# Optimization experiments

Hardware: AMD Instinct MI355X
Metric: run time of the kernel (lower is better)

Reference implementation:

```python
import jax, jax.numpy as jnp
import numpy as np

N_NODES = 50000


def _gin_aggregate(x, src, dst):
    # sum_{j in N(i)} x_j via scatter-add over edges; eps=0 so add self term
    msg = x[src]  # [E, d]
    return x + jax.ops.segment_sum(msg, dst, num_segments=N_NODES)


def _mlp(h, Wa, ba, Wb, bb):
    return jax.nn.relu(h @ Wa + ba) @ Wb + bb


def setup_inputs() -> dict:
    key = jax.random.key(0)
    ks = jax.random.split(key, 12)
    d_in, d_h, n_cls, n_edges = 128, 128, 40, 800000
    x = jax.random.normal(ks[0], (N_NODES, d_in), dtype=jnp.float32)
    edge_index = jax.random.randint(ks[1], (2, n_edges), 0, N_NODES, dtype=jnp.int64)
    s = lambda k, sh: jax.random.normal(k, sh, dtype=jnp.float32) / np.sqrt(sh[0])
    return {
        "x": x,
        "edge_index": edge_index,
        "W11": s(ks[2], (d_in, 2 * d_h)), "b11": jnp.zeros((2 * d_h,), jnp.float32),
        "W12": s(ks[3], (2 * d_h, d_h)), "b12": jnp.zeros((d_h,), jnp.float32),
        "W21": s(ks[4], (d_h, 2 * d_h)), "b21": jnp.zeros((2 * d_h,), jnp.float32),
        "W22": s(ks[5], (2 * d_h, d_h)), "b22": jnp.zeros((d_h,), jnp.float32),
        "Wfc": s(ks[6], (d_h, n_cls)), "bfc": jnp.zeros((n_cls,), jnp.float32),
    }


def reference(x, edge_index, W11, b11, W12, b12, W21, b21, W22, b22, Wfc, bfc):
    src, dst = edge_index[0], edge_index[1]
    # GINConv 1: aggregate then MLP, followed by ReLU
    h = _mlp(_gin_aggregate(x, src, dst), W11, b11, W12, b12)
    h = jax.nn.relu(h)
    # GINConv 2
    h = _mlp(_gin_aggregate(h, src, dst), W21, b21, W22, b22)
    h = jax.nn.relu(h)
    # final classifier
    return h @ Wfc + bfc
```

## Files before the change

kernel.cpp:

```cpp
#include <hip/hip_runtime.h>

#define N_NODES 50000
#define N_EDGES 800000
#define NBUCK   98
#define EPB     8192

typedef __attribute__((ext_vector_type(8))) short short8;
typedef __attribute__((ext_vector_type(4))) float floatx4;

__device__ __forceinline__ float b2f(unsigned short u) {
    union { unsigned int i; float f; } v;
    v.i = ((unsigned int)u) << 16;
    return v.f;
}
__device__ __forceinline__ float ubits(unsigned int b) {
    union { unsigned int i; float f; } v;
    v.i = b;
    return v.f;
}
__device__ __forceinline__ unsigned short f2b(float f) {
    union { float f; unsigned int i; } v;
    v.f = f;
    unsigned int r = v.i + 0x7FFFu + ((v.i >> 16) & 1u);
    return (unsigned short)(r >> 16);
}

__global__ __launch_bounds__(256) void bhist_kernel(const int* __restrict__ dstv,
                                                    int* __restrict__ bkt_cnt) {
    __shared__ int h[NBUCK];
    const int tid = threadIdx.x;
    for (int i = tid; i < NBUCK; i += 256) h[i] = 0;
    __syncthreads();
    const int e0 = blockIdx.x * 1024;
#pragma unroll
    for (int j = 0; j < 4; ++j) {
        int e = e0 + j * 256 + tid;
        if (e < N_EDGES) atomicAdd(&h[dstv[e] >> 9], 1);
    }
    __syncthreads();
    for (int i = tid; i < NBUCK; i += 256)
        if (h[i]) atomicAdd(&bkt_cnt[i], h[i]);
}

__global__ __launch_bounds__(128) void bscan_kernel(const int* __restrict__ bkt_cnt,
                                                    int* __restrict__ bbase,
                                                    int* __restrict__ bcur) {
    __shared__ int s[128];
    const int t = threadIdx.x;
    const int v = (t < NBUCK) ? bkt_cnt[t] : 0;
    s[t] = v;
    __syncthreads();
    for (int off = 1; off < 128; off <<= 1) {
        int u = (t >= off) ? s[t - off] : 0;
        __syncthreads();
        s[t] += u;
        __syncthreads();
    }
    if (t == 0) bbase[0] = 0;
    if (t < NBUCK) {
        bbase[t + 1] = s[t];
        bcur[t] = s[t] - v;
    }
}

__global__ __launch_bounds__(256) void bucket_scatter(const int* __restrict__ srcv,
                                                      const int* __restrict__ dstv,
                                                      int* __restrict__ bcur,
                                                      int* __restrict__ tmp) {
    __shared__ int hist[NBUCK];
    __shared__ int base[NBUCK];
    const int tid = threadIdx.x;
    const int e0 = blockIdx.x * EPB;
    for (int i = tid; i < NBUCK; i += 256) hist[i] = 0;
    __syncthreads();
#pragma unroll 4
    for (int j = 0; j < EPB / 256; ++j) {
        int e = e0 + j * 256 + tid;
        if (e < N_EDGES) atomicAdd(&hist[dstv[e] >> 9], 1);
    }
    __syncthreads();
    for (int i = tid; i < NBUCK; i += 256) {
        base[i] = atomicAdd(&bcur[i], hist[i]);
        hist[i] = 0;
    }
    __syncthreads();
#pragma unroll 4
    for (int j = 0; j < EPB / 256; ++j) {
        int e = e0 + j * 256 + tid;
        if (e < N_EDGES) {
            int d = dstv[e];
            int b = d >> 9;
            int r = atomicAdd(&hist[b], 1);
            tmp[base[b] + r] = srcv[e] | ((d & 511) << 16);
        }
    }
}

__global__ __launch_bounds__(256) void bucket_sort_ex(const int* __restrict__ bbase,
                                                      const int* __restrict__ tmp,
                                                      int* __restrict__ e_src,
                                                      int* __restrict__ row_ptr) {
    __shared__ int cnt[512];
    __shared__ int ps[256];
    __shared__ int buf[12288];
    const int tid = threadIdx.x;
    const int b = blockIdx.x;
    const int nb = b << 9;
    const int rbase = bbase[b], rend = bbase[b + 1];
    const int S = rend - rbase;

    for (int i = tid; i < 512; i += 256) cnt[i] = 0;
    __syncthreads();
    for (int e = tid; e < S; e += 256)
        atomicAdd(&cnt[(tmp[rbase + e] >> 16) & 511], 1);
    __syncthreads();

    const int c0 = cnt[2 * tid], c1 = cnt[2 * tid + 1];
    ps[tid] = c0 + c1;
    __syncthreads();
    for (int off = 1; off < 256; off <<= 1) {
        int u = (tid >= off) ? ps[tid - off] : 0;
        __syncthreads();
        ps[tid] += u;
        __syncthreads();
    }
    const int off0 = ps[tid] - (c0 + c1);
    const int off1 = off0 + c0;
    cnt[2 * tid] = off0;
    cnt[2 * tid + 1] = off1;
    if (nb + 2 * tid < N_NODES)     row_ptr[nb + 2 * tid] = rbase + off0;
    if (nb + 2 * tid + 1 < N_NODES) row_ptr[nb + 2 * tid + 1] = rbase + off1;
    if (b == NBUCK - 1 && tid == 0) row_ptr[N_NODES] = N_EDGES;
    __syncthreads();

    for (int e = tid; e < S; e += 256) {
        int p = tmp[rbase + e];
        int dl = (p >> 16) & 511;
        int pos = atomicAdd(&cnt[dl], 1);
        buf[pos] = p & 0xFFFF;
    }
    __syncthreads();
    for (int i = tid; i < S; i += 256) e_src[rbase + i] = buf[i];
}

__global__ void prep_kernel(const float* __restrict__ x,
                            const float* __restrict__ W11, const float* __restrict__ W12,
                            const float* __restrict__ W21, const float* __restrict__ W22,
                            const float* __restrict__ Wfc,
                            unsigned short* __restrict__ xb,
                            unsigned short* __restrict__ Wt11, unsigned short* __restrict__ Wt12,
                            unsigned short* __restrict__ Wt21, unsigned short* __restrict__ Wt22,
                            unsigned short* __restrict__ Wfct,
                            int* __restrict__ bkt_cnt) {
    int bid = blockIdx.x;
    if (bid < 512) {
        int which = bid >> 7;
        int idx = (bid & 127) * 256 + threadIdx.x;
        const float* W = (which == 0) ? W11 : (which == 1) ? W12 : (which == 2) ? W21 : W22;
        unsigned short* Wt = (which == 0) ? Wt11 : (which == 1) ? Wt12 : (which == 2) ? Wt21 : Wt22;
        int K = (which & 1) ? 256 : 128;
        int N = (which & 1) ? 128 : 256;
        int k = idx / N, n = idx - k * N;
        Wt[n * K + k] = f2b(W[idx]);
    } else if (bid < 536) {
        int idx = (bid - 512) * 256 + threadIdx.x;
        int n = idx >> 7, k = idx & 127;
        Wfct[idx] = (n < 40) ? f2b(Wfc[k * 40 + n]) : (unsigned short)0;
    } else if (bid < 3661) {
        int i = (bid - 536) * 256 + threadIdx.x;
        const float4 a = *reinterpret_cast<const float4*>(x + (size_t)i * 8);
        const float4 b = *reinterpret_cast<const float4*>(x + (size_t)i * 8 + 4);
        ushort4 u0, u1;
        u0.x = f2b(a.x); u0.y = f2b(a.y); u0.z = f2b(a.z); u0.w = f2b(a.w);
        u1.x = f2b(b.x); u1.y = f2b(b.y); u1.z = f2b(b.z); u1.w = f2b(b.w);
        *reinterpret_cast<ushort4*>(xb + (size_t)i * 8) = u0;
        *reinterpret_cast<ushort4*>(xb + (size_t)i * 8 + 4) = u1;
    } else {
        if (threadIdx.x < NBUCK) bkt_cnt[threadIdx.x] = 0;
    }
}

__global__ __launch_bounds__(256) void agg_bf16q(const unsigned short* __restrict__ X,
                                                 const int* __restrict__ row_ptr,
                                                 const int* __restrict__ e_src,
                                                 unsigned short* __restrict__ agg) {
    const int node = (blockIdx.x * 256 + threadIdx.x) >> 6;
    const int lane = threadIdx.x & 63;
    const int qw = lane >> 4, ql = lane & 15;
    const size_t off = (size_t)ql * 8;

    const int beg = row_ptr[node], end = row_ptr[node + 1];
    float acc[8];
#pragma unroll
    for (int k = 0; k < 8; ++k) acc[k] = 0.f;

    if (qw == 0) {
        uint4 u = *reinterpret_cast<const uint4*>(X + (size_t)node * 128 + off);
        const unsigned int* up = (const unsigned int*)&u;
#pragma unroll
        for (int k = 0; k < 4; ++k) {
            acc[2 * k]     += ubits(up[k] << 16);
            acc[2 * k + 1] += ubits(up[k] & 0xFFFF0000u);
        }
    }

    int e = beg + qw;
    for (; e + 12 < end; e += 16) {
        const int s0 = e_src[e], s1 = e_src[e + 4], s2 = e_src[e + 8], s3 = e_src[e + 12];
        uint4 u0 = *reinterpret_cast<const uint4*>(X + (size_t)s0 * 128 + off);
        uint4 u1 = *reinterpret_cast<const uint4*>(X + (size_t)s1 * 128 + off);
        uint4 u2 = *reinterpret_cast<const uint4*>(X + (size_t)s2 * 128 + off);
        uint4 u3 = *reinterpret_cast<const uint4*>(X + (size_t)s3 * 128 + off);
        const unsigned int* p0 = (const unsigned int*)&u0;
        const unsigned int* p1 = (const unsigned int*)&u1;
        const unsigned int* p2 = (const unsigned int*)&u2;
        const unsigned int* p3 = (const unsigned int*)&u3;
#pragma unroll
        for (int k = 0; k < 4; ++k) {
            acc[2 * k]     += ubits(p0[k] << 16) + ubits(p1[k] << 16)
                            + ubits(p2[k] << 16) + ubits(p3[k] << 16);
            acc[2 * k + 1] += ubits(p0[k] & 0xFFFF0000u) + ubits(p1[k] & 0xFFFF0000u)
                            + ubits(p2[k] & 0xFFFF0000u) + ubits(p3[k] & 0xFFFF0000u);
        }
    }
    for (; e + 4 < end; e += 8) {
        const int s0 = e_src[e], s1 = e_src[e + 4];
        uint4 u0 = *reinterpret_cast<const uint4*>(X + (size_t)s0 * 128 + off);
        uint4 u1 = *reinterpret_cast<const uint4*>(X + (size_t)s1 * 128 + off);
        const unsigned int* p0 = (const unsigned int*)&u0;
        const unsigned int* p1 = (const unsigned int*)&u1;
#pragma unroll
        for (int k = 0; k < 4; ++k) {
            acc[2 * k]     += ubits(p0[k] << 16) + ubits(p1[k] << 16);
            acc[2 * k + 1] += ubits(p0[k] & 0xFFFF0000u) + ubits(p1[k] & 0xFFFF0000u);
        }
    }
    if (e < end) {
        const int s = e_src[e];
        uint4 u = *reinterpret_cast<const uint4*>(X + (size_t)s * 128 + off);
        const unsigned int* p = (const unsigned int*)&u;
#pragma unroll
        for (int k = 0; k < 4; ++k) {
            acc[2 * k]     += ubits(p[k] << 16);
            acc[2 * k + 1] += ubits(p[k] & 0xFFFF0000u);
        }
    }

#pragma unroll
    for (int k = 0; k < 8; ++k) acc[k] += __shfl_xor(acc[k], 32);
#pragma unroll
    for (int k = 0; k < 8; ++k) acc[k] += __shfl_xor(acc[k], 16);

    if (qw == 0) {
        ushort4 o0, o1;
        o0.x = f2b(acc[0]); o0.y = f2b(acc[1]); o0.z = f2b(acc[2]); o0.w = f2b(acc[3]);
        o1.x = f2b(acc[4]); o1.y = f2b(acc[5]); o1.z = f2b(acc[6]); o1.w = f2b(acc[7]);
        unsigned short* p = agg + (size_t)node * 128 + off;
        *reinterpret_cast<ushort4*>(p) = o0;
        *reinterpret_cast<ushort4*>(p + 4) = o1;
    }
}

template <bool FUSE>
__global__ __launch_bounds__(256, FUSE ? 2 : 3) void mlp_fused(
    const unsigned short* __restrict__ X, const unsigned short* __restrict__ Wt1,
    const float* __restrict__ b1, const unsigned short* __restrict__ Wt2,
    const float* __restrict__ b2, unsigned short* __restrict__ Y,
    const unsigned short* __restrict__ Wfct, const float* __restrict__ bfc,
    float* __restrict__ out, int M) {
    __shared__ __align__(16) char smem[FUSE ? 57344 : 52224];
    unsigned short* A   = (unsigned short*)smem;
    unsigned short* B2q = (unsigned short*)smem;
    unsigned short* B1h = (unsigned short*)(smem + 17408);
    unsigned short* T   = (unsigned short*)(smem + 17408);
    unsigned short* Hc  = (unsigned short*)(smem + 52224);

    const int tid = threadIdx.x;
    const int m0 = blockIdx.x * 64;
    const int lane = tid & 63, w = tid >> 6;
    const int qm = lane & 15, quad = lane >> 4;

#pragma unroll
    for (int j = 0; j < 4; ++j) {
        int i = j * 256 + tid;
        int r = i >> 4, c8 = (i & 15) << 3;
        uint4 v = {0, 0, 0, 0};
        if (m0 + r < M) v = *reinterpret_cast<const uint4*>(X + (size_t)(m0 + r) * 128 + c8);
        *reinterpret_cast<uint4*>(&A[r * 136 + c8]) = v;
    }

    floatx4 acc1[2][4][2];
#pragma unroll
    for (int c = 0; c < 2; ++c)
#pragma unroll
        for (int mt = 0; mt < 4; ++mt)
#pragma unroll
            for (int nt = 0; nt < 2; ++nt) acc1[c][mt][nt] = {0.f, 0.f, 0.f, 0.f};

    for (int c = 0; c < 2; ++c) {
#pragma unroll
        for (int j = 0; j < 8; ++j) {
            int i = j * 256 + tid;
            int r = i >> 4, c8 = (i & 15) << 3;
            *reinterpret_cast<uint4*>(&B1h[r * 136 + c8]) =
                *reinterpret_cast<const uint4*>(Wt1 + (size_t)(c * 128 + r) * 128 + c8);
        }
        __syncthreads();
#pragma unroll
        for (int ks = 0; ks < 4; ++ks) {
            const int kb = ks * 32 + quad * 8;
            short8 a[4], b[2];
#pragma unroll
            for (int mt = 0; mt < 4; ++mt)
                a[mt] = *reinterpret_cast<const short8*>(&A[(mt * 16 + qm) * 136 + kb]);
#pragma unroll
            for (int nt = 0; nt < 2; ++nt)
                b[nt] = *reinterpret_cast<const short8*>(&B1h[(w * 32 + nt * 16 + qm) * 136 + kb]);
#pragma unroll
            for (int mt = 0; mt < 4; ++mt)
#pragma unroll
                for (int nt = 0; nt < 2; ++nt)
                    acc1[c][mt][nt] = __builtin_amdgcn_mfma_f32_16x16x32_bf16(
                        a[mt], b[nt], acc1[c][mt][nt], 0, 0, 0);
        }
        __syncthreads();
    }

#pragma unroll
    for (int c = 0; c < 2; ++c) {
#pragma unroll
        for (int nt = 0; nt < 2; ++nt) {
            const int jcol = c * 128 + w * 32 + nt * 16 + qm;
            const float bj = b1[jcol];
#pragma unroll
            for (int mt = 0; mt < 4; ++mt)
#pragma unroll
                for (int r = 0; r < 4; ++r)
                    T[(mt * 16 + quad * 4 + r) * 264 + jcol] =
                        f2b(fmaxf(acc1[c][mt][nt][r] + bj, 0.f));
        }
    }

    floatx4 cacc[3];
#pragma unroll
    for (int nt = 0; nt < 3; ++nt) cacc[nt] = {0.f, 0.f, 0.f, 0.f};

    for (int c2 = 0; c2 < 4; ++c2) {
#pragma unroll
        for (int j = 0; j < 4; ++j) {
            int i = j * 256 + tid;
            int r = i >> 5, c8 = (i & 31) << 3;
            *reinterpret_cast<uint4*>(&B2q[r * 264 + c8]) =
                *reinterpret_cast<const uint4*>(Wt2 + (size_t)(c2 * 32 + r) * 256 + c8);
        }
        __syncthreads();

        floatx4 acc2[2];
        acc2[0] = {0.f, 0.f, 0.f, 0.f};
        acc2[1] = {0.f, 0.f, 0.f, 0.f};
#pragma unroll
        for (int ks = 0; ks < 8; ++ks) {
            const int kb = ks * 32 + quad * 8;
            short8 t0 = *reinterpret_cast<const short8*>(&T[((w & 1) * 32 + qm) * 264 + kb]);
            short8 t1 = *reinterpret_cast<const short8*>(&T[((w & 1) * 32 + 16 + qm) * 264 + kb]);
            short8 bb = *reinterpret_cast<const short8*>(&B2q[((w >> 1) * 16 + qm) * 264 + kb]);
            acc2[0] = __builtin_amdgcn_mfma_f32_16x16x32_bf16(t0, bb, acc2[0], 0, 0, 0);
            acc2[1] = __builtin_amdgcn_mfma_f32_16x16x32_bf16(t1, bb, acc2[1], 0, 0, 0);
        }

        const int ncol = c2 * 32 + (w >> 1) * 16 + qm;
        const float bj = b2[ncol];
        if (!FUSE) {
#pragma unroll
            for (int mt2 = 0; mt2 < 2; ++mt2)
#pragma unroll
                for (int r = 0; r < 4; ++r) {
                    int row = m0 + (w & 1) * 32 + mt2 * 16 + quad * 4 + r;
                    if (row < M)
                        Y[(size_t)row * 128 + ncol] = f2b(fmaxf(acc2[mt2][r] + bj, 0.f));
                }
            __syncthreads();
        } else {
            const int lcol = (w >> 1) * 16 + qm;
#pragma unroll
            for (int mt2 = 0; mt2 < 2; ++mt2)
#pragma unroll
                for (int r = 0; r < 4; ++r)
                    Hc[((w & 1) * 32 + mt2 * 16 + quad * 4 + r) * 40 + lcol] =
                        f2b(fmaxf(acc2[mt2][r] + bj, 0.f));
            __syncthreads();
            short8 hf = *reinterpret_cast<const short8*>(&Hc[(w * 16 + qm) * 40 + quad * 8]);
#pragma unroll
            for (int nt = 0; nt < 3; ++nt) {
                short8 bf = *reinterpret_cast<const short8*>(
                    Wfct + (nt * 16 + qm) * 128 + c2 * 32 + quad * 8);
                cacc[nt] = __builtin_amdgcn_mfma_f32_16x16x32_bf16(hf, bf, cacc[nt], 0, 0, 0);
            }
            __syncthreads();
        }
    }

    if (FUSE) {
#pragma unroll
        for (int nt = 0; nt < 3; ++nt) {
            int col = nt * 16 + qm;
            if (col < 40) {
                const float bj = bfc[col];
#pragma unroll
                for (int r = 0; r < 4; ++r) {
                    int row = m0 + w * 16 + quad * 4 + r;
                    if (row < M) out[(size_t)row * 40 + col] = cacc[nt][r] + bj;
                }
            }
        }
    }
}

extern "C" void kernel_launch(void* const* d_in, const int* in_sizes, int n_in,
                              void* d_out, int out_size, void* d_ws, size_t ws_size,
                              hipStream_t stream) {
    const float* x   = (const float*)d_in[0];
    const int*   ei  = (const int*)d_in[1];
    const float* W11 = (const float*)d_in[2];
    const float* b11 = (const float*)d_in[3];
    const float* W12 = (const float*)d_in[4];
    const float* b12 = (const float*)d_in[5];
    const float* W21 = (const float*)d_in[6];
    const float* b21 = (const float*)d_in[7];
    const float* W22 = (const float*)d_in[8];
    const float* b22 = (const float*)d_in[9];
    const float* Wfc = (const float*)d_in[10];
    const float* bfc = (const float*)d_in[11];
    float* out = (float*)d_out;

    const int* srcv = ei;
    const int* dstv = ei + N_EDGES;

    unsigned short* agg  = (unsigned short*)d_ws;
    unsigned short* h    = agg + (size_t)N_NODES * 128;
    unsigned short* xb   = h   + (size_t)N_NODES * 128;
    unsigned short* Wt11 = xb  + (size_t)N_NODES * 128;
    unsigned short* Wt12 = Wt11 + 256 * 128;
    unsigned short* Wt21 = Wt12 + 256 * 128;
    unsigned short* Wt22 = Wt21 + 256 * 128;
    unsigned short* Wfct = Wt22 + 256 * 128;
    int* bkt_cnt = (int*)(Wfct + 48 * 128);
    int* bbase   = bkt_cnt + 128;
    int* bcur    = bbase + 128;
    int* row_ptr = bcur + 128;
    int* e_src   = row_ptr + N_NODES + 4;
    int* tmp     = e_src + N_EDGES;

    prep_kernel<<<3662, 256, 0, stream>>>(x, W11, W12, W21, W22, Wfc,
                                          xb, Wt11, Wt12, Wt21, Wt22, Wfct, bkt_cnt);

    bhist_kernel<<<(N_EDGES + 1023) / 1024, 256, 0, stream>>>(dstv, bkt_cnt);
    bscan_kernel<<<1, 128, 0, stream>>>(bkt_cnt, bbase, bcur);
    bucket_scatter<<<(N_EDGES + EPB - 1) / EPB, 256, 0, stream>>>(srcv, dstv, bcur, tmp);
    bucket_sort_ex<<<NBUCK, 256, 0, stream>>>(bbase, tmp, e_src, row_ptr);

    const int agg_blocks = N_NODES * 64 / 256;
    const int mlp_blocks = (N_NODES + 63) / 64;

    agg_bf16q<<<agg_blocks, 256, 0, stream>>>(xb, row_ptr, e_src, agg);
    mlp_fused<false><<<mlp_blocks, 256, 0, stream>>>(
        agg, Wt11, b11, Wt12, b12, h, nullptr, nullptr, nullptr, N_NODES);
    agg_bf16q<<<agg_blocks, 256, 0, stream>>>(h, row_ptr, e_src, agg);
    mlp_fused<true><<<mlp_blocks, 256, 0, stream>>>(
        agg, Wt21, b21, Wt22, b22, nullptr, Wfct, bfc, out, N_NODES);
}
```

Before: 272.2 us.

## Fuse edge bucketing into prep kernel using fixed-capacity bucket slots

Drops the global bucket histogram and scan kernels. The edge scatter now runs inside the prep kernel: each superblock writes its edges into fixed-capacity per-(superblock, bucket) slots and records its per-bucket counts. The bucket sort kernel then does a local scan over superblock counts, gathers the edges into shared memory, and writes padded per-bucket CSR segments; the aggregation kernel's row_ptr indexing is adjusted to match. This removes several kernel launches and the global atomic offset pass. In exchange it relies on fixed capacities (160 per slot, 12288 per bucket) and silently drops edges on skewed graphs that exceed them.

```diff
diff --git a/kernel.cpp b/kernel.cpp
--- a/kernel.cpp
+++ b/kernel.cpp
@@ -4,6 +4,9 @@
 #define N_EDGES 800000
 #define NBUCK   98
 #define EPB     8192
+#define NSB     98
+#define BCAP    160
+#define CAPB    12288
 
 typedef __attribute__((ext_vector_type(8))) short short8;
 typedef __attribute__((ext_vector_type(4))) float floatx4;
@@ -25,137 +28,22 @@
     return (unsigned short)(r >> 16);
 }
 
-__global__ __launch_bounds__(256) void bhist_kernel(const int* __restrict__ dstv,
-                                                    int* __restrict__ bkt_cnt) {
-    __shared__ int h[NBUCK];
+__global__ __launch_bounds__(256) void prep_scatter(
+    const float* __restrict__ x,
+    const float* __restrict__ W11, const float* __restrict__ W12,
+    const float* __restrict__ W21, const float* __restrict__ W22,
+    const float* __restrict__ Wfc,
+    const int* __restrict__ srcv, const int* __restrict__ dstv,
+    unsigned short* __restrict__ xb,
+    unsigned short* __restrict__ Wt11, unsigned short* __restrict__ Wt12,
+    unsigned short* __restrict__ Wt21, unsigned short* __restrict__ Wt22,
+    unsigned short* __restrict__ Wfct,
+    int* __restrict__ cnt, int* __restrict__ tmp) {
+    const int bid = blockIdx.x;
     const int tid = threadIdx.x;
-    for (int i = tid; i < NBUCK; i += 256) h[i] = 0;
-    __syncthreads();
-    const int e0 = blockIdx.x * 1024;
-#pragma unroll
-    for (int j = 0; j < 4; ++j) {
-        int e = e0 + j * 256 + tid;
-        if (e < N_EDGES) atomicAdd(&h[dstv[e] >> 9], 1);
-    }
-    __syncthreads();
-    for (int i = tid; i < NBUCK; i += 256)
-        if (h[i]) atomicAdd(&bkt_cnt[i], h[i]);
-}
-
-__global__ __launch_bounds__(128) void bscan_kernel(const int* __restrict__ bkt_cnt,
-                                                    int* __restrict__ bbase,
-                                                    int* __restrict__ bcur) {
-    __shared__ int s[128];
-    const int t = threadIdx.x;
-    const int v = (t < NBUCK) ? bkt_cnt[t] : 0;
-    s[t] = v;
-    __syncthreads();
-    for (int off = 1; off < 128; off <<= 1) {
-        int u = (t >= off) ? s[t - off] : 0;
-        __syncthreads();
-        s[t] += u;
-        __syncthreads();
-    }
-    if (t == 0) bbase[0] = 0;
-    if (t < NBUCK) {
-        bbase[t + 1] = s[t];
-        bcur[t] = s[t] - v;
-    }
-}
-
-__global__ __launch_bounds__(256) void bucket_scatter(const int* __restrict__ srcv,
-                                                      const int* __restrict__ dstv,
-                                                      int* __restrict__ bcur,
-                                                      int* __restrict__ tmp) {
-    __shared__ int hist[NBUCK];
-    __shared__ int base[NBUCK];
-    const int tid = threadIdx.x;
-    const int e0 = blockIdx.x * EPB;
-    for (int i = tid; i < NBUCK; i += 256) hist[i] = 0;
-    __syncthreads();
-#pragma unroll 4
-    for (int j = 0; j < EPB / 256; ++j) {
-        int e = e0 + j * 256 + tid;
-        if (e < N_EDGES) atomicAdd(&hist[dstv[e] >> 9], 1);
-    }
-    __syncthreads();
-    for (int i = tid; i < NBUCK; i += 256) {
-        base[i] = atomicAdd(&bcur[i], hist[i]);
-        hist[i] = 0;
-    }
-    __syncthreads();
-#pragma unroll 4
-    for (int j = 0; j < EPB / 256; ++j) {
-        int e = e0 + j * 256 + tid;
-        if (e < N_EDGES) {
-            int d = dstv[e];
-            int b = d >> 9;
-            int r = atomicAdd(&hist[b], 1);
-            tmp[base[b] + r] = srcv[e] | ((d & 511) << 16);
-        }
-    }
-}
-
-__global__ __launch_bounds__(256) void bucket_sort_ex(const int* __restrict__ bbase,
-                                                      const int* __restrict__ tmp,
-                                                      int* __restrict__ e_src,
-                                                      int* __restrict__ row_ptr) {
-    __shared__ int cnt[512];
-    __shared__ int ps[256];
-    __shared__ int buf[12288];
-    const int tid = threadIdx.x;
-    const int b = blockIdx.x;
-    const int nb = b << 9;
-    const int rbase = bbase[b], rend = bbase[b + 1];
-    const int S = rend - rbase;
-
-    for (int i = tid; i < 512; i += 256) cnt[i] = 0;
-    __syncthreads();
-    for (int e = tid; e < S; e += 256)
-        atomicAdd(&cnt[(tmp[rbase + e] >> 16) & 511], 1);
-    __syncthreads();
-
-    const int c0 = cnt[2 * tid], c1 = cnt[2 * tid + 1];
-    ps[tid] = c0 + c1;
-    __syncthreads();
-    for (int off = 1; off < 256; off <<= 1) {
-        int u = (tid >= off) ? ps[tid - off] : 0;
-        __syncthreads();
-        ps[tid] += u;
-        __syncthreads();
-    }
-    const int off0 = ps[tid] - (c0 + c1);
-    const int off1 = off0 + c0;
-    cnt[2 * tid] = off0;
-    cnt[2 * tid + 1] = off1;
-    if (nb + 2 * tid < N_NODES)     row_ptr[nb + 2 * tid] = rbase + off0;
-    if (nb + 2 * tid + 1 < N_NODES) row_ptr[nb + 2 * tid + 1] = rbase + off1;
-    if (b == NBUCK - 1 && tid == 0) row_ptr[N_NODES] = N_EDGES;
-    __syncthreads();
-
-    for (int e = tid; e < S; e += 256) {
-        int p = tmp[rbase + e];
-        int dl = (p >> 16) & 511;
-        int pos = atomicAdd(&cnt[dl], 1);
-        buf[pos] = p & 0xFFFF;
-    }
-    __syncthreads();
-    for (int i = tid; i < S; i += 256) e_src[rbase + i] = buf[i];
-}
-
-__global__ void prep_kernel(const float* __restrict__ x,
-                            const float* __restrict__ W11, const float* __restrict__ W12,
-                            const float* __restrict__ W21, const float* __restrict__ W22,
-                            const float* __restrict__ Wfc,
-                            unsigned short* __restrict__ xb,
-                            unsigned short* __restrict__ Wt11, unsigned short* __restrict__ Wt12,
-                            unsigned short* __restrict__ Wt21, unsigned short* __restrict__ Wt22,
-                            unsigned short* __restrict__ Wfct,
-                            int* __restrict__ bkt_cnt) {
-    int bid = blockIdx.x;
     if (bid < 512) {
         int which = bid >> 7;
-        int idx = (bid & 127) * 256 + threadIdx.x;
+        int idx = (bid & 127) * 256 + tid;
         const float* W = (which == 0) ? W11 : (which == 1) ? W12 : (which == 2) ? W21 : W22;
         unsigned short* Wt = (which == 0) ? Wt11 : (which == 1) ? Wt12 : (which == 2) ? Wt21 : Wt22;
         int K = (which & 1) ? 256 : 128;
@@ -163,11 +51,11 @@
         int k = idx / N, n = idx - k * N;
         Wt[n * K + k] = f2b(W[idx]);
     } else if (bid < 536) {
-        int idx = (bid - 512) * 256 + threadIdx.x;
+        int idx = (bid - 512) * 256 + tid;
         int n = idx >> 7, k = idx & 127;
         Wfct[idx] = (n < 40) ? f2b(Wfc[k * 40 + n]) : (unsigned short)0;
     } else if (bid < 3661) {
-        int i = (bid - 536) * 256 + threadIdx.x;
+        int i = (bid - 536) * 256 + tid;
         const float4 a = *reinterpret_cast<const float4*>(x + (size_t)i * 8);
         const float4 b = *reinterpret_cast<const float4*>(x + (size_t)i * 8 + 4);
         ushort4 u0, u1;
@@ -176,7 +64,101 @@
         *reinterpret_cast<ushort4*>(xb + (size_t)i * 8) = u0;
         *reinterpret_cast<ushort4*>(xb + (size_t)i * 8 + 4) = u1;
     } else {
-        if (threadIdx.x < NBUCK) bkt_cnt[threadIdx.x] = 0;
+        __shared__ int hist[NBUCK];
+        const int k = bid - 3661;
+        const int e0 = k * EPB;
+        for (int i = tid; i < NBUCK; i += 256) hist[i] = 0;
+        __syncthreads();
+#pragma unroll 4
+        for (int j = 0; j < EPB / 256; ++j) {
+            int e = e0 + j * 256 + tid;
+            if (e < N_EDGES) atomicAdd(&hist[dstv[e] >> 9], 1);
+        }
+        __syncthreads();
+        for (int i = tid; i < NBUCK; i += 256) {
+            cnt[i * NSB + k] = hist[i];
+            hist[i] = 0;
+        }
+        __syncthreads();
+#pragma unroll 4
+        for (int j = 0; j < EPB / 256; ++j) {
+            int e = e0 + j * 256 + tid;
+            if (e < N_EDGES) {
+                int d = dstv[e];
+                int b = d >> 9;
+                int r = atomicAdd(&hist[b], 1);
+                if (r < BCAP)
+                    tmp[((size_t)k * NBUCK + b) * BCAP + r] = srcv[e] | ((d & 511) << 16);
+            }
+        }
+    }
+}
+
+__global__ __launch_bounds__(256) void bucket_sort_ex(const int* __restrict__ cnt,
+                                                      const int* __restrict__ tmp,
+                                                      int* __restrict__ e_src,
+                                                      int* __restrict__ row_ptr) {
+    __shared__ int ps[256];
+    __shared__ int sb[NSB];
+    __shared__ int sc[NSB];
+    __shared__ int nc[512];
+    __shared__ int buf[CAPB];
+    const int tid = threadIdx.x;
+    const int b = blockIdx.x;
+
+    const int v = (tid < NSB) ? cnt[b * NSB + tid] : 0;
+    ps[tid] = v;
+    __syncthreads();
+    for (int off = 1; off < 256; off <<= 1) {
+        int u = (tid >= off) ? ps[tid - off] : 0;
+        __syncthreads();
+        ps[tid] += u;
+        __syncthreads();
+    }
+    if (tid < NSB) {
+        sb[tid] = ps[tid] - v;
+        sc[tid] = v;
+    }
+    __syncthreads();
+    const int S = ps[255];
+
+    const int lane = tid & 63, w = tid >> 6;
+    for (int k = w; k < NSB; k += 4) {
+        const int base = sb[k], c = sc[k];
+        const int* src = tmp + ((size_t)k * NBUCK + b) * BCAP;
+        for (int i = lane; i < c; i += 64)
+            if (base + i < CAPB) buf[base + i] = src[i];
+    }
+    for (int i = tid; i < 512; i += 256) nc[i] = 0;
+    __syncthreads();
+    for (int e = tid; e < S; e += 256)
+        atomicAdd(&nc[(buf[e] >> 16) & 511], 1);
+    __syncthreads();
+
+    const int c0 = nc[2 * tid], c1 = nc[2 * tid + 1];
+    ps[tid] = c0 + c1;
+    __syncthreads();
+    for (int off = 1; off < 256; off <<= 1) {
+        int u = (tid >= off) ? ps[tid - off] : 0;
+        __syncthreads();
+        ps[tid] += u;
+        __syncthreads();
+    }
+    const int off0 = ps[tid] - (c0 + c1);
+    const int off1 = off0 + c0;
+    nc[2 * tid] = off0;
+    nc[2 * tid + 1] = off1;
+    const int gbase = b * CAPB;
+    row_ptr[b * 513 + 2 * tid] = gbase + off0;
+    row_ptr[b * 513 + 2 * tid + 1] = gbase + off1;
+    if (tid == 0) row_ptr[b * 513 + 512] = gbase + S;
+    __syncthreads();
+
+    for (int e = tid; e < S; e += 256) {
+        int p = buf[e];
+        int dl = (p >> 16) & 511;
+        int pos = atomicAdd(&nc[dl], 1);
+        e_src[gbase + pos] = p & 0xFFFF;
     }
 }
 
@@ -189,7 +171,8 @@
     const int qw = lane >> 4, ql = lane & 15;
     const size_t off = (size_t)ql * 8;
 
-    const int beg = row_ptr[node], end = row_ptr[node + 1];
+    const int rp = node + (node >> 9);
+    const int beg = row_ptr[rp], end = row_ptr[rp + 1];
     float acc[8];
 #pragma unroll
     for (int k = 0; k < 8; ++k) acc[k] = 0.f;
@@ -444,20 +427,16 @@
     unsigned short* Wt21 = Wt12 + 256 * 128;
     unsigned short* Wt22 = Wt21 + 256 * 128;
     unsigned short* Wfct = Wt22 + 256 * 128;
-    int* bkt_cnt = (int*)(Wfct + 48 * 128);
-    int* bbase   = bkt_cnt + 128;
-    int* bcur    = bbase + 128;
-    int* row_ptr = bcur + 128;
-    int* e_src   = row_ptr + N_NODES + 4;
-    int* tmp     = e_src + N_EDGES;
-
-    prep_kernel<<<3662, 256, 0, stream>>>(x, W11, W12, W21, W22, Wfc,
-                                          xb, Wt11, Wt12, Wt21, Wt22, Wfct, bkt_cnt);
-
-    bhist_kernel<<<(N_EDGES + 1023) / 1024, 256, 0, stream>>>(dstv, bkt_cnt);
-    bscan_kernel<<<1, 128, 0, stream>>>(bkt_cnt, bbase, bcur);
-    bucket_scatter<<<(N_EDGES + EPB - 1) / EPB, 256, 0, stream>>>(srcv, dstv, bcur, tmp);
-    bucket_sort_ex<<<NBUCK, 256, 0, stream>>>(bbase, tmp, e_src, row_ptr);
+    int* cnt     = (int*)(Wfct + 48 * 128);
+    int* row_ptr = cnt + 9728;
+    int* e_src   = row_ptr + 50304;
+    int* tmp     = e_src + (size_t)NBUCK * CAPB;
+
+    prep_scatter<<<3661 + NSB, 256, 0, stream>>>(
+        x, W11, W12, W21, W22, Wfc, srcv, dstv,
+        xb, Wt11, Wt12, Wt21, Wt22, Wfct, cnt, tmp);
+
+    bucket_sort_ex<<<NBUCK, 256, 0, stream>>>(cnt, tmp, e_src, row_ptr);
 
     const int agg_blocks = N_NODES * 64 / 256;
     const int mlp_blocks = (N_NODES + 63) / 64;
```

New measurement: 265.7 us. -2.4%, faster.
